# Kernel tuning notes

Hardware: AMD Instinct MI355X
Metric: run time of the kernel (lower is better)

Reference implementation:

```python
import jax, jax.numpy as jnp
import numpy as np

EPS = 1e-8

def mlp(x, w1, b1, w2, b2):
    return jnp.tanh(x @ w1 + b1) @ w2 + b2

def setup_inputs() -> dict:
    key = jax.random.key(0)
    ks = jax.random.split(key, 24)
    N_NEWS, N_USERS, N_ATR = 50000, 100000, 1000
    E_ATR, E_USR = 100000, 2000000
    D = 768
    def lin(k, fi, fo):
        return jax.random.normal(k, (fi, fo), jnp.float32) * (1.0 / np.sqrt(fi))
    inp = {
        'news_x': jax.random.normal(ks[0], (N_NEWS, D), jnp.float32),
        'users_x': jax.random.normal(ks[1], (N_USERS, 128), jnp.float32),
        'w1a': lin(ks[2], D, 256), 'b1a': jnp.zeros((256,), jnp.float32),
        'w1b': lin(ks[3], 256, 128), 'b1b': jnp.zeros((128,), jnp.float32),
        'wna': lin(ks[4], D + 128, 512), 'bna': jnp.zeros((512,), jnp.float32),
        'wnb': lin(ks[5], 512, 128), 'bnb': jnp.zeros((128,), jnp.float32),
        'wua': lin(ks[6], 256, 256), 'bua': jnp.zeros((256,), jnp.float32),
        'wub': lin(ks[7], 256, 128), 'bub': jnp.zeros((128,), jnp.float32),
        'atr_row': jax.random.randint(ks[8], (E_ATR,), 0, N_NEWS, jnp.int32),
        'atr_col': jax.random.randint(ks[9], (E_ATR,), 0, N_ATR, jnp.int32),
        'usr_row': jax.random.randint(ks[10], (E_USR,), 0, N_NEWS, jnp.int32),
        'usr_col': jax.random.randint(ks[11], (E_USR,), 0, N_USERS, jnp.int32),
        'n_news': N_NEWS, 'n_users': N_USERS, 'n_atr': N_ATR,
    }
    return inp

def reference(news_x, users_x, w1a, b1a, w1b, b1b, wna, bna, wnb, bnb,
              wua, bua, wub, bub, atr_row, atr_col, usr_row, usr_col,
              n_news, n_users, n_atr):
    dt = news_x.dtype
    ones_a = jnp.ones(atr_row.shape[0], dt)
    ones_u = jnp.ones(usr_row.shape[0], dt)
    # FirstConv: news -> attribute nodes (edge_index.t() @ news)
    deg_atr = jax.ops.segment_sum(ones_a, atr_col, num_segments=n_atr)
    agr_atr = jax.ops.segment_sum(news_x[atr_row], atr_col, num_segments=n_atr)
    agr_atr = agr_atr / (deg_atr[:, None] + EPS)
    atr_feats = mlp(agr_atr, w1a, b1a, w1b, b1b)  # [n_atr, 128]
    # NewsConv: attribute -> news (edge_index @ atr_feats), concat with news_x
    deg_news = jax.ops.segment_sum(ones_a, atr_row, num_segments=n_news)
    agr_news = jax.ops.segment_sum(atr_feats[atr_col], atr_row, num_segments=n_news)
    agr_news = agr_news / (deg_news[:, None] + EPS)
    news_out = mlp(jnp.concatenate([news_x, agr_news], axis=1), wna, bna, wnb, bnb)  # [n_news,128]
    # UserConv: news -> users (edge_index['users'].t() @ news), concat with users_x
    deg_usr = jax.ops.segment_sum(ones_u, usr_col, num_segments=n_users)
    agr_usr = jax.ops.segment_sum(news_out[usr_row], usr_col, num_segments=n_users)
    agr_usr = agr_usr / (deg_usr[:, None] + EPS)
    users_out = mlp(jnp.concatenate([users_x, agr_usr], axis=1), wua, bua, wub, bub)  # [n_users,128]
    # stack final news + user embeddings into one array
    return jnp.concatenate([news_out, users_out], axis=0)  # [n_news+n_users, 128]
```

## Files before the change

kernel.cpp:

```cpp
#include <hip/hip_runtime.h>

#define N_NEWS 50000
#define N_USERS 100000
#define N_ATR 1000
#define E_ATR 100000
#define E_USR 2000000
#define NTOT (N_ATR + N_NEWS + N_USERS)
#define EPSF 1e-8f

#define ACAP 192
#define NCAP 24
#define UCAP 64
#define FCH 8192

typedef short s16x8 __attribute__((ext_vector_type(8)));
typedef float f32x4 __attribute__((ext_vector_type(4)));

__device__ inline ushort f2bf(float f) {
    uint u = __float_as_uint(f);
    u += 0x7fffu + ((u >> 16) & 1u);
    return (ushort)(u >> 16);
}
__device__ inline float bflo(uint v) { return __uint_as_float(v << 16); }
__device__ inline float bfhi(uint v) { return __uint_as_float(v & 0xffff0000u); }
__device__ inline float fast_tanh(float x) {
    x = fminf(fmaxf(x, -15.0f), 15.0f);
    float e = __expf(2.0f * x);
    return (e - 1.0f) / (e + 1.0f);
}

struct TrJob { const float* src; ushort* dst; int R, C, blkEnd; };

struct PrepArgs {
    const int *atr_row, *atr_col, *usr_row, *usr_col;
    int *cnt_atr, *cnt_news, *cnt_usr;
    int *ids_atr, *ids_news, *ids_usr;
    const float *news_x, *users_x;
    ushort *news_bf, *users_bf;
    int fu, fa, tr, n1, n2;
    TrJob j[6];
};

__global__ void prep_k(PrepArgs A) {
    __shared__ float tile[32][33];
    int b = blockIdx.x;
    int t = threadIdx.x;
    if (b < A.fu) {
        int part = b & 7;
        int chunk = b >> 3;
        int lo = part * (N_USERS / 8), hi = lo + (N_USERS / 8);
        int base = chunk * FCH;
        int endE = base + FCH; if (endE > E_USR) endE = E_USR;
        for (int e = base + t; e < endE; e += 256) {
            int c = A.usr_col[e];
            int r = A.usr_row[e];
            if (c >= lo && c < hi) {
                int slot = atomicAdd(&A.cnt_usr[c], 1);
                if (slot < UCAP) A.ids_usr[(size_t)c * UCAP + slot] = r;
            }
        }
        return;
    }
    b -= A.fu;
    if (b < A.fa) {
        int total = 2 * E_ATR;
        int per = (total + A.fa - 1) / A.fa;
        int base = b * per;
        int endE = base + per; if (endE > total) endE = total;
        for (int e = base + t; e < endE; e += 256) {
            if (e < E_ATR) {
                int c = A.atr_col[e];
                int slot = atomicAdd(&A.cnt_atr[c], 1);
                if (slot < ACAP) A.ids_atr[(size_t)c * ACAP + slot] = A.atr_row[e];
            } else {
                int e2 = e - E_ATR;
                int r = A.atr_row[e2];
                int slot = atomicAdd(&A.cnt_news[r], 1);
                if (slot < NCAP) A.ids_news[(size_t)r * NCAP + slot] = A.atr_col[e2];
            }
        }
        return;
    }
    b -= A.fa;
    if (b < A.tr) {
        int ji = 0;
        while (b >= A.j[ji].blkEnd) ++ji;
        const TrJob& J = A.j[ji];
        int lb = b - (ji ? A.j[ji - 1].blkEnd : 0);
        int ctiles = J.C / 32;
        int bc = (lb % ctiles) * 32, br = (lb / ctiles) * 32;
        int tx = t & 31, ty = t >> 5;
        for (int i = 0; i < 4; ++i)
            tile[ty + i * 8][tx] = J.src[(size_t)(br + ty + i * 8) * J.C + bc + tx];
        __syncthreads();
        for (int i = 0; i < 4; ++i)
            J.dst[(size_t)(bc + ty + i * 8) * J.R + br + tx] = f2bf(tile[tx][ty + i * 8]);
        return;
    }
    b -= A.tr;
    int i = b * 256 + t;
    const float* src; ushort* dst;
    if (i < A.n1) { src = A.news_x; dst = A.news_bf; }
    else          { i -= A.n1; if (i >= A.n2) return; src = A.users_x; dst = A.users_bf; }
    const float4* p = (const float4*)src + (size_t)i * 2;
    float4 a = p[0], c4 = p[1];
    uint4 v;
    v.x = (uint)f2bf(a.x) | ((uint)f2bf(a.y) << 16);
    v.y = (uint)f2bf(a.z) | ((uint)f2bf(a.w) << 16);
    v.z = (uint)f2bf(c4.x) | ((uint)f2bf(c4.y) << 16);
    v.w = (uint)f2bf(c4.z) | ((uint)f2bf(c4.w) << 16);
    ((uint4*)dst)[i] = v;
}

__global__ void gather768b_k(const ushort* __restrict__ src, const int* __restrict__ ids,
                             const int* __restrict__ cnt, ushort* __restrict__ agr_b) {
    int u = blockIdx.x;
    int t = threadIdx.x;
    int dc = cnt[u];
    int d = dc < ACAP ? dc : ACAP;
    const int* bp = ids + (size_t)u * ACAP;
    float a0 = 0.f, a1 = 0.f, a2 = 0.f, a3 = 0.f;
    int i = 0;
    for (; i + 3 < d; i += 4) {
        const uint* r0 = (const uint*)(src + (size_t)bp[i] * 768);
        const uint* r1 = (const uint*)(src + (size_t)bp[i + 1] * 768);
        const uint* r2 = (const uint*)(src + (size_t)bp[i + 2] * 768);
        const uint* r3 = (const uint*)(src + (size_t)bp[i + 3] * 768);
        uint v0 = r0[t], v1 = r1[t], v2 = r2[t], v3 = r3[t];
        a0 += bflo(v0) + bflo(v1) + bflo(v2) + bflo(v3);
        a1 += bfhi(v0) + bfhi(v1) + bfhi(v2) + bfhi(v3);
        if (t < 128) {
            uint w0 = r0[t + 256], w1 = r1[t + 256], w2 = r2[t + 256], w3 = r3[t + 256];
            a2 += bflo(w0) + bflo(w1) + bflo(w2) + bflo(w3);
            a3 += bfhi(w0) + bfhi(w1) + bfhi(w2) + bfhi(w3);
        }
    }
    for (; i < d; ++i) {
        const uint* r0 = (const uint*)(src + (size_t)bp[i] * 768);
        uint v0 = r0[t];
        a0 += bflo(v0); a1 += bfhi(v0);
        if (t < 128) {
            uint v1 = r0[t + 256];
            a2 += bflo(v1); a3 += bfhi(v1);
        }
    }
    float inv = 1.0f / ((float)dc + EPSF);
    uint* dst = (uint*)(agr_b + (size_t)u * 768);
    dst[t] = (uint)f2bf(a0 * inv) | ((uint)f2bf(a1 * inv) << 16);
    if (t < 128)
        dst[256 + t] = (uint)f2bf(a2 * inv) | ((uint)f2bf(a3 * inv) << 16);
}

template<int CAP>
__global__ void gather128c_k(const ushort* __restrict__ srcp, const int* __restrict__ ids,
                             const int* __restrict__ cnt, ushort* __restrict__ agr, int n) {
    int u = blockIdx.x * 4 + (threadIdx.x >> 6);
    if (u >= n) return;
    int lane = threadIdx.x & 63;
    int dc = cnt[u];
    int d = dc < CAP ? dc : CAP;
    const int* bp = ids + (size_t)u * CAP;
    float ax = 0.f, ay = 0.f;
    int i = 0;
    for (; i + 3 < d; i += 4) {
        int s0 = bp[i], s1 = bp[i + 1], s2 = bp[i + 2], s3 = bp[i + 3];
        uint v0 = ((const uint*)srcp)[(size_t)s0 * 64 + lane];
        uint v1 = ((const uint*)srcp)[(size_t)s1 * 64 + lane];
        uint v2 = ((const uint*)srcp)[(size_t)s2 * 64 + lane];
        uint v3 = ((const uint*)srcp)[(size_t)s3 * 64 + lane];
        ax += bflo(v0) + bflo(v1) + bflo(v2) + bflo(v3);
        ay += bfhi(v0) + bfhi(v1) + bfhi(v2) + bfhi(v3);
    }
    for (; i < d; ++i) {
        uint v0 = ((const uint*)srcp)[(size_t)bp[i] * 64 + lane];
        ax += bflo(v0); ay += bfhi(v0);
    }
    float inv = 1.0f / ((float)dc + EPSF);
    uint packed = (uint)f2bf(ax * inv) | ((uint)f2bf(ay * inv) << 16);
    *(uint*)(agr + (size_t)u * 128 + lane * 2) = packed;
}

template<int NS, int NS1, bool TANH, int OMODE, int GY>
__launch_bounds__(256, 3)
__global__ void gemm5_k(const ushort* __restrict__ A1, const ushort* __restrict__ A2,
                        const ushort* __restrict__ Bt, const float* __restrict__ bias,
                        float* __restrict__ outf, ushort* __restrict__ outb,
                        int M, int N) {
    __shared__ __align__(16) char lds[32768];
    const int t = threadIdx.x;
    const int w = t >> 6, l = t & 63, lr = l & 15, lk = l >> 4;
    const int wm = w >> 1, wn = w & 1;
    int nwg = gridDim.x;
    int q = nwg >> 3, r = nwg & 7;
    int xcd = blockIdx.x & 7, idx = blockIdx.x >> 3;
    int fid = (xcd < r) ? xcd * (q + 1) + idx : r * (q + 1) + (xcd - r) * q + idx;
    constexpr int LG = (GY == 4) ? 2 : (GY == 2) ? 1 : 0;
    const int row0 = (fid >> LG) * 128;
    const int col0 = (fid & (GY - 1)) * 128;
    constexpr int A1RB = NS1 * 128;
    constexpr int A2RB = (NS - NS1) * 128;
    constexpr int BRB = NS * 128;

    auto stage = [&](int s) {
        const char* abase; int arb, soff;
        if (s < NS1) { abase = (const char*)A1; arb = A1RB; soff = s * 128; }
        else         { abase = (const char*)A2; arb = A2RB; soff = (s - NS1) * 128; }
#pragma unroll
        for (int i = 0; i < 4; ++i) {
            int chunk = i * 256 + w * 64 + l;
            int row = chunk >> 3, sub = chunk & 7;
            int rg = row0 + row; if (rg >= M) rg = M - 1;
            const char* src = abase + (size_t)rg * arb + soff + ((sub * 16) ^ ((row & 7) << 4));
            __builtin_amdgcn_global_load_lds(
                (const __attribute__((address_space(1))) unsigned int*)src,
                (__attribute__((address_space(3))) unsigned int*)(lds + i * 4096 + w * 1024),
                16, 0, 0);
        }
#pragma unroll
        for (int i = 0; i < 4; ++i) {
            int chunk = i * 256 + w * 64 + l;
            int row = chunk >> 3, sub = chunk & 7;
            const char* src = (const char*)Bt + (size_t)(col0 + row) * BRB + s * 128
                              + ((sub * 16) ^ ((row & 7) << 4));
            __builtin_amdgcn_global_load_lds(
                (const __attribute__((address_space(1))) unsigned int*)src,
                (__attribute__((address_space(3))) unsigned int*)(lds + 16384 + i * 4096 + w * 1024),
                16, 0, 0);
        }
    };

    f32x4 acc[4][4];
#pragma unroll
    for (int i = 0; i < 4; ++i)
#pragma unroll
        for (int j = 0; j < 4; ++j) acc[i][j] = (f32x4)0.f;

    stage(0);
    for (int s = 0; s < NS; ++s) {
        __syncthreads();
#pragma unroll
        for (int ks = 0; ks < 2; ++ks) {
            s16x8 af[4], bf[4];
#pragma unroll
            for (int rt = 0; rt < 4; ++rt) {
                int rr = wm * 64 + rt * 16 + lr;
                af[rt] = *(const s16x8*)(lds + rr * 128 + ((ks * 64 + lk * 16) ^ ((rr & 7) << 4)));
            }
#pragma unroll
            for (int ct = 0; ct < 4; ++ct) {
                int c = wn * 64 + ct * 16 + lr;
                bf[ct] = *(const s16x8*)(lds + 16384 + c * 128 + ((ks * 64 + lk * 16) ^ ((c & 7) << 4)));
            }
#pragma unroll
            for (int rt = 0; rt < 4; ++rt)
#pragma unroll
                for (int ct = 0; ct < 4; ++ct)
                    acc[rt][ct] = __builtin_amdgcn_mfma_f32_16x16x32_bf16(
                        af[rt], bf[ct], acc[rt][ct], 0, 0, 0);
        }
        __syncthreads();
        if (s + 1 < NS) stage(s + 1);
    }

    if (OMODE == 0) {
#pragma unroll
        for (int rt = 0; rt < 4; ++rt)
#pragma unroll
            for (int ct = 0; ct < 4; ++ct) {
                int c = wn * 64 + ct * 16 + lr;
                float bs = bias[col0 + c];
#pragma unroll
                for (int r4 = 0; r4 < 4; ++r4) {
                    int rr = wm * 64 + rt * 16 + lk * 4 + r4;
                    float v = acc[rt][ct][r4] + bs;
                    if (TANH) v = fast_tanh(v);
                    *(ushort*)(lds + rr * 256 + ((c * 2) ^ ((rr & 7) << 4))) = f2bf(v);
                }
            }
        __syncthreads();
#pragma unroll
        for (int i = 0; i < 8; ++i) {
            int chunk = i * 256 + t;
            int rr = chunk >> 4, cb = (chunk & 15) * 16;
            int rg = row0 + rr;
            if (rg < M)
                *(float4*)((char*)outb + (size_t)rg * (N * 2) + col0 * 2 + cb) =
                    *(const float4*)(lds + rr * 256 + (cb ^ ((rr & 7) << 4)));
        }
    } else {
#pragma unroll
        for (int rt = 0; rt < 4; ++rt)
#pragma unroll
            for (int ct = 0; ct < 4; ++ct) {
                int c = col0 + wn * 64 + ct * 16 + lr;
                float bs = bias[c];
#pragma unroll
                for (int r4 = 0; r4 < 4; ++r4) {
                    int rg = row0 + wm * 64 + rt * 16 + lk * 4 + r4;
                    if (rg < M) {
                        float v = acc[rt][ct][r4] + bs;
                        if (TANH) v = fast_tanh(v);
                        outf[(size_t)rg * N + c] = v;
                        if (OMODE == 2) outb[(size_t)rg * N + c] = f2bf(v);
                    }
                }
            }
    }
}

extern "C" void kernel_launch(void* const* d_in, const int* in_sizes, int n_in,
                              void* d_out, int out_size, void* d_ws, size_t ws_size,
                              hipStream_t stream) {
    const float* news_x  = (const float*)d_in[0];
    const float* users_x = (const float*)d_in[1];
    const float* w1a = (const float*)d_in[2];
    const float* b1a = (const float*)d_in[3];
    const float* w1b = (const float*)d_in[4];
    const float* b1b = (const float*)d_in[5];
    const float* wna = (const float*)d_in[6];
    const float* bna = (const float*)d_in[7];
    const float* wnb = (const float*)d_in[8];
    const float* bnb = (const float*)d_in[9];
    const float* wua = (const float*)d_in[10];
    const float* bua = (const float*)d_in[11];
    const float* wub = (const float*)d_in[12];
    const float* bub = (const float*)d_in[13];
    const int* atr_row = (const int*)d_in[14];
    const int* atr_col = (const int*)d_in[15];
    const int* usr_row = (const int*)d_in[16];
    const int* usr_col = (const int*)d_in[17];

    char* ws = (char*)d_ws;
    size_t o = 0;
    auto alloc = [&](size_t bytes) { void* p = ws + o; o += (bytes + 255) & ~(size_t)255; return p; };

    int* cnt_all = (int*)alloc((size_t)NTOT * 4);
    size_t zero_bytes = o;
    int* cnt_atr  = cnt_all;
    int* cnt_news = cnt_all + N_ATR;
    int* cnt_usr  = cnt_all + N_ATR + N_NEWS;
    int* ids_atr  = (int*)alloc((size_t)N_ATR * ACAP * 4);
    int* ids_news = (int*)alloc((size_t)N_NEWS * NCAP * 4);
    int* ids_usr  = (int*)alloc((size_t)N_USERS * UCAP * 4);
    ushort* news_bf    = (ushort*)alloc((size_t)N_NEWS * 768 * 2);
    ushort* users_bf   = (ushort*)alloc((size_t)N_USERS * 128 * 2);
    ushort* agr_atr_b  = (ushort*)alloc((size_t)N_ATR * 768 * 2);
    ushort* h_atr_b    = (ushort*)alloc((size_t)N_ATR * 256 * 2);
    ushort* atr_feats_b= (ushort*)alloc((size_t)N_ATR * 128 * 2);
    ushort* agr_news_b = (ushort*)alloc((size_t)N_NEWS * 128 * 2);
    ushort* agr_usr_b  = (ushort*)alloc((size_t)N_USERS * 128 * 2);
    ushort* out_news_b = (ushort*)alloc((size_t)N_NEWS * 128 * 2);
    ushort* h_buf      = (ushort*)alloc((size_t)N_USERS * 256 * 2);
    ushort* w1at = (ushort*)alloc((size_t)256 * 768 * 2);
    ushort* w1bt = (ushort*)alloc((size_t)128 * 256 * 2);
    ushort* wnat = (ushort*)alloc((size_t)512 * 896 * 2);
    ushort* wnbt = (ushort*)alloc((size_t)128 * 512 * 2);
    ushort* wuat = (ushort*)alloc((size_t)256 * 256 * 2);
    ushort* wubt = (ushort*)alloc((size_t)128 * 256 * 2);

    float* out = (float*)d_out;
    float* out_users = out + (size_t)N_NEWS * 128;

    hipMemsetAsync(cnt_all, 0, zero_bytes, stream);

    {
        PrepArgs A;
        A.atr_row = atr_row; A.atr_col = atr_col;
        A.usr_row = usr_row; A.usr_col = usr_col;
        A.cnt_atr = cnt_atr; A.cnt_news = cnt_news; A.cnt_usr = cnt_usr;
        A.ids_atr = ids_atr; A.ids_news = ids_news; A.ids_usr = ids_usr;
        A.news_x = news_x; A.users_x = users_x;
        A.news_bf = news_bf; A.users_bf = users_bf;
        A.fu = ((E_USR + FCH - 1) / FCH) * 8;
        A.fa = 25;
        A.n1 = N_NEWS * 768 / 8;
        A.n2 = N_USERS * 128 / 8;
        int acc2 = 0;
        auto add = [&](int i, const float* s, ushort* d, int R, int C) {
            acc2 += (C / 32) * (R / 32);
            A.j[i] = TrJob{s, d, R, C, acc2};
        };
        add(0, w1a, w1at, 768, 256);
        add(1, w1b, w1bt, 256, 128);
        add(2, wna, wnat, 896, 512);
        add(3, wnb, wnbt, 512, 128);
        add(4, wua, wuat, 256, 256);
        add(5, wub, wubt, 256, 128);
        A.tr = acc2;
        int cvt_blk = (A.n1 + A.n2 + 255) / 256;
        prep_k<<<A.fu + A.fa + A.tr + cvt_blk, 256, 0, stream>>>(A);
    }

    gather768b_k<<<N_ATR, 256, 0, stream>>>(news_bf, ids_atr, cnt_atr, agr_atr_b);
    gemm5_k<12, 12, true, 0, 2><<<16, 256, 0, stream>>>(
        agr_atr_b, nullptr, w1at, b1a, nullptr, h_atr_b, N_ATR, 256);
    gemm5_k<4, 4, false, 0, 1><<<8, 256, 0, stream>>>(
        h_atr_b, nullptr, w1bt, b1b, nullptr, atr_feats_b, N_ATR, 128);
    gather128c_k<NCAP><<<(N_NEWS + 3) / 4, 256, 0, stream>>>(
        atr_feats_b, ids_news, cnt_news, agr_news_b, N_NEWS);

    gemm5_k<14, 12, true, 0, 4><<<391 * 4, 256, 0, stream>>>(
        news_bf, agr_news_b, wnat, bna, nullptr, h_buf, N_NEWS, 512);
    gemm5_k<8, 8, false, 2, 1><<<391, 256, 0, stream>>>(
        h_buf, nullptr, wnbt, bnb, out, out_news_b, N_NEWS, 128);

    gather128c_k<UCAP><<<(N_USERS + 3) / 4, 256, 0, stream>>>(
        out_news_b, ids_usr, cnt_usr, agr_usr_b, N_USERS);
    gemm5_k<4, 2, true, 0, 2><<<782 * 2, 256, 0, stream>>>(
        users_bf, agr_usr_b, wuat, bua, nullptr, h_buf, N_USERS, 256);
    gemm5_k<4, 4, false, 1, 1><<<782, 256, 0, stream>>>(
        h_buf, nullptr, wubt, bub, out_users, nullptr, N_USERS, 128);
}
```

Before: 468.3 us.

## Replace per-user atomic bucketing with two-level partitioned CSR build for user edges

The user-edge bucketing no longer scans all 2M edges eight times with a global atomic per user. Edges are first binned into 250 partitions using block-local shared-memory counters, with one global atomic per partition per block. A new mid kernel then counting-sorts each partition into a compact CSR (start/count), and runs alongside the 768-wide attribute gather. This cuts redundant edge reads and global atomic contention, but adds a packed 64-bit arena pass and an extra kernel phase, and relies on a fixed per-partition capacity.

```diff
diff --git a/kernel.cpp b/kernel.cpp
--- a/kernel.cpp
+++ b/kernel.cpp
@@ -5,13 +5,14 @@
 #define N_ATR 1000
 #define E_ATR 100000
 #define E_USR 2000000
-#define NTOT (N_ATR + N_NEWS + N_USERS)
 #define EPSF 1e-8f
 
 #define ACAP 192
 #define NCAP 24
-#define UCAP 64
-#define FCH 8192
+#define P_USR 250
+#define UPP 400
+#define ACAPP 9216
+#define EBLK_A 8192
 
 typedef short s16x8 __attribute__((ext_vector_type(8)));
 typedef float f32x4 __attribute__((ext_vector_type(4)));
@@ -33,35 +34,46 @@
 
 struct PrepArgs {
     const int *atr_row, *atr_col, *usr_row, *usr_col;
-    int *cnt_atr, *cnt_news, *cnt_usr;
-    int *ids_atr, *ids_news, *ids_usr;
+    int *cnt_atr, *cnt_news, *arena_cnt;
+    int *ids_atr, *ids_news;
+    unsigned long long* arena;
     const float *news_x, *users_x;
     ushort *news_bf, *users_bf;
-    int fu, fa, tr, n1, n2;
+    int pa, fa, tr, n1, n2;
     TrJob j[6];
 };
 
 __global__ void prep_k(PrepArgs A) {
     __shared__ float tile[32][33];
+    __shared__ int cloc[P_USR], cbase[P_USR];
     int b = blockIdx.x;
     int t = threadIdx.x;
-    if (b < A.fu) {
-        int part = b & 7;
-        int chunk = b >> 3;
-        int lo = part * (N_USERS / 8), hi = lo + (N_USERS / 8);
-        int base = chunk * FCH;
-        int endE = base + FCH; if (endE > E_USR) endE = E_USR;
+    if (b < A.pa) {
+        if (t < P_USR) cloc[t] = 0;
+        __syncthreads();
+        int base = b * EBLK_A;
+        int endE = base + EBLK_A; if (endE > E_USR) endE = E_USR;
+        for (int e = base + t; e < endE; e += 256)
+            atomicAdd(&cloc[A.usr_col[e] / UPP], 1);
+        __syncthreads();
+        if (t < P_USR) {
+            cbase[t] = atomicAdd(&A.arena_cnt[t], cloc[t]);
+            cloc[t] = 0;
+        }
+        __syncthreads();
         for (int e = base + t; e < endE; e += 256) {
             int c = A.usr_col[e];
             int r = A.usr_row[e];
-            if (c >= lo && c < hi) {
-                int slot = atomicAdd(&A.cnt_usr[c], 1);
-                if (slot < UCAP) A.ids_usr[(size_t)c * UCAP + slot] = r;
-            }
+            int p = c / UPP;
+            int off = atomicAdd(&cloc[p], 1);
+            int slot = cbase[p] + off;
+            if (slot < ACAPP)
+                A.arena[(size_t)p * ACAPP + slot] =
+                    ((unsigned long long)(uint)c << 32) | (uint)r;
         }
         return;
     }
-    b -= A.fu;
+    b -= A.pa;
     if (b < A.fa) {
         int total = 2 * E_ATR;
         int per = (total + A.fa - 1) / A.fa;
@@ -112,13 +124,61 @@
     ((uint4*)dst)[i] = v;
 }
 
-__global__ void gather768b_k(const ushort* __restrict__ src, const int* __restrict__ ids,
-                             const int* __restrict__ cnt, ushort* __restrict__ agr_b) {
-    int u = blockIdx.x;
+struct MidArgs {
+    const unsigned long long* arena;
+    const int* arena_cnt;
+    int *cnt_usr, *start_usr, *ids_usr;
+    const ushort* news_bf;
+    const int* ids_atr;
+    const int* cnt_atr;
+    ushort* agr_atr_b;
+};
+
+__global__ void mid_k(MidArgs M) {
+    __shared__ int cnt[512];
+    __shared__ int scn[512];
+    int b = blockIdx.x;
     int t = threadIdx.x;
-    int dc = cnt[u];
+    if (b < P_USR) {
+        int p = b;
+        int nA = M.arena_cnt[p]; if (nA > ACAPP) nA = ACAPP;
+        const unsigned long long* ar = M.arena + (size_t)p * ACAPP;
+        cnt[t] = 0; cnt[t + 256] = 0;
+        __syncthreads();
+        for (int i = t; i < nA; i += 256)
+            atomicAdd(&cnt[(int)(ar[i] >> 32) - p * UPP], 1);
+        __syncthreads();
+        scn[t] = cnt[t]; scn[t + 256] = cnt[t + 256];
+        __syncthreads();
+        for (int off = 1; off < 512; off <<= 1) {
+            int v0 = (t >= off) ? scn[t - off] : 0;
+            int v1 = ((t + 256) >= off) ? scn[t + 256 - off] : 0;
+            __syncthreads();
+            scn[t] += v0; scn[t + 256] += v1;
+            __syncthreads();
+        }
+        for (int i = t; i < UPP; i += 256) {
+            int u = p * UPP + i;
+            M.cnt_usr[u] = cnt[i];
+            M.start_usr[u] = p * ACAPP + (scn[i] - cnt[i]);
+        }
+        __syncthreads();
+        for (int i = t; i < UPP; i += 256) cnt[i] = scn[i] - cnt[i];
+        __syncthreads();
+        for (int i = t; i < nA; i += 256) {
+            unsigned long long v = ar[i];
+            int c = (int)(v >> 32);
+            int off = atomicAdd(&cnt[c - p * UPP], 1);
+            M.ids_usr[(size_t)p * ACAPP + off] = (int)(v & 0xffffffffu);
+        }
+        return;
+    }
+    b -= P_USR;
+    int u = b;
+    int dc = M.cnt_atr[u];
     int d = dc < ACAP ? dc : ACAP;
-    const int* bp = ids + (size_t)u * ACAP;
+    const int* bp = M.ids_atr + (size_t)u * ACAP;
+    const ushort* src = M.news_bf;
     float a0 = 0.f, a1 = 0.f, a2 = 0.f, a3 = 0.f;
     int i = 0;
     for (; i + 3 < d; i += 4) {
@@ -145,7 +205,7 @@
         }
     }
     float inv = 1.0f / ((float)dc + EPSF);
-    uint* dst = (uint*)(agr_b + (size_t)u * 768);
+    uint* dst = (uint*)(M.agr_atr_b + (size_t)u * 768);
     dst[t] = (uint)f2bf(a0 * inv) | ((uint)f2bf(a1 * inv) << 16);
     if (t < 128)
         dst[256 + t] = (uint)f2bf(a2 * inv) | ((uint)f2bf(a3 * inv) << 16);
@@ -176,6 +236,34 @@
         ax += bflo(v0); ay += bfhi(v0);
     }
     float inv = 1.0f / ((float)dc + EPSF);
+    uint packed = (uint)f2bf(ax * inv) | ((uint)f2bf(ay * inv) << 16);
+    *(uint*)(agr + (size_t)u * 128 + lane * 2) = packed;
+}
+
+__global__ void gather128s_k(const ushort* __restrict__ srcp, const int* __restrict__ ids,
+                             const int* __restrict__ start, const int* __restrict__ cnt,
+                             ushort* __restrict__ agr, int n) {
+    int u = blockIdx.x * 4 + (threadIdx.x >> 6);
+    if (u >= n) return;
+    int lane = threadIdx.x & 63;
+    int d = cnt[u];
+    const int* bp = ids + start[u];
+    float ax = 0.f, ay = 0.f;
+    int i = 0;
+    for (; i + 3 < d; i += 4) {
+        int s0 = bp[i], s1 = bp[i + 1], s2 = bp[i + 2], s3 = bp[i + 3];
+        uint v0 = ((const uint*)srcp)[(size_t)s0 * 64 + lane];
+        uint v1 = ((const uint*)srcp)[(size_t)s1 * 64 + lane];
+        uint v2 = ((const uint*)srcp)[(size_t)s2 * 64 + lane];
+        uint v3 = ((const uint*)srcp)[(size_t)s3 * 64 + lane];
+        ax += bflo(v0) + bflo(v1) + bflo(v2) + bflo(v3);
+        ay += bfhi(v0) + bfhi(v1) + bfhi(v2) + bfhi(v3);
+    }
+    for (; i < d; ++i) {
+        uint v0 = ((const uint*)srcp)[(size_t)bp[i] * 64 + lane];
+        ax += bflo(v0); ay += bfhi(v0);
+    }
+    float inv = 1.0f / ((float)d + EPSF);
     uint packed = (uint)f2bf(ax * inv) | ((uint)f2bf(ay * inv) << 16);
     *(uint*)(agr + (size_t)u * 128 + lane * 2) = packed;
 }
@@ -334,14 +422,16 @@
     size_t o = 0;
     auto alloc = [&](size_t bytes) { void* p = ws + o; o += (bytes + 255) & ~(size_t)255; return p; };
 
-    int* cnt_all = (int*)alloc((size_t)NTOT * 4);
+    int* cnt_atr   = (int*)alloc(N_ATR * 4);
+    int* cnt_news  = (int*)alloc(N_NEWS * 4);
+    int* arena_cnt = (int*)alloc(P_USR * 4);
     size_t zero_bytes = o;
-    int* cnt_atr  = cnt_all;
-    int* cnt_news = cnt_all + N_ATR;
-    int* cnt_usr  = cnt_all + N_ATR + N_NEWS;
+    int* cnt_usr   = (int*)alloc((size_t)N_USERS * 4);
+    int* start_usr = (int*)alloc((size_t)N_USERS * 4);
     int* ids_atr  = (int*)alloc((size_t)N_ATR * ACAP * 4);
     int* ids_news = (int*)alloc((size_t)N_NEWS * NCAP * 4);
-    int* ids_usr  = (int*)alloc((size_t)N_USERS * UCAP * 4);
+    int* ids_usr  = (int*)alloc((size_t)P_USR * ACAPP * 4);
+    unsigned long long* arena = (unsigned long long*)alloc((size_t)P_USR * ACAPP * 8);
     ushort* news_bf    = (ushort*)alloc((size_t)N_NEWS * 768 * 2);
     ushort* users_bf   = (ushort*)alloc((size_t)N_USERS * 128 * 2);
     ushort* agr_atr_b  = (ushort*)alloc((size_t)N_ATR * 768 * 2);
@@ -361,17 +451,18 @@
     float* out = (float*)d_out;
     float* out_users = out + (size_t)N_NEWS * 128;
 
-    hipMemsetAsync(cnt_all, 0, zero_bytes, stream);
+    hipMemsetAsync(cnt_atr, 0, zero_bytes, stream);
 
     {
         PrepArgs A;
         A.atr_row = atr_row; A.atr_col = atr_col;
         A.usr_row = usr_row; A.usr_col = usr_col;
-        A.cnt_atr = cnt_atr; A.cnt_news = cnt_news; A.cnt_usr = cnt_usr;
-        A.ids_atr = ids_atr; A.ids_news = ids_news; A.ids_usr = ids_usr;
+        A.cnt_atr = cnt_atr; A.cnt_news = cnt_news; A.arena_cnt = arena_cnt;
+        A.ids_atr = ids_atr; A.ids_news = ids_news;
+        A.arena = arena;
         A.news_x = news_x; A.users_x = users_x;
         A.news_bf = news_bf; A.users_bf = users_bf;
-        A.fu = ((E_USR + FCH - 1) / FCH) * 8;
+        A.pa = (E_USR + EBLK_A - 1) / EBLK_A;
         A.fa = 25;
         A.n1 = N_NEWS * 768 / 8;
         A.n2 = N_USERS * 128 / 8;
@@ -388,10 +479,18 @@
         add(5, wub, wubt, 256, 128);
         A.tr = acc2;
         int cvt_blk = (A.n1 + A.n2 + 255) / 256;
-        prep_k<<<A.fu + A.fa + A.tr + cvt_blk, 256, 0, stream>>>(A);
-    }
-
-    gather768b_k<<<N_ATR, 256, 0, stream>>>(news_bf, ids_atr, cnt_atr, agr_atr_b);
+        prep_k<<<A.pa + A.fa + A.tr + cvt_blk, 256, 0, stream>>>(A);
+    }
+
+    {
+        MidArgs M;
+        M.arena = arena; M.arena_cnt = arena_cnt;
+        M.cnt_usr = cnt_usr; M.start_usr = start_usr; M.ids_usr = ids_usr;
+        M.news_bf = news_bf; M.ids_atr = ids_atr; M.cnt_atr = cnt_atr;
+        M.agr_atr_b = agr_atr_b;
+        mid_k<<<P_USR + N_ATR, 256, 0, stream>>>(M);
+    }
+
     gemm5_k<12, 12, true, 0, 2><<<16, 256, 0, stream>>>(
         agr_atr_b, nullptr, w1at, b1a, nullptr, h_atr_b, N_ATR, 256);
     gemm5_k<4, 4, false, 0, 1><<<8, 256, 0, stream>>>(
@@ -404,8 +503,8 @@
     gemm5_k<8, 8, false, 2, 1><<<391, 256, 0, stream>>>(
         h_buf, nullptr, wnbt, bnb, out, out_news_b, N_NEWS, 128);
 
-    gather128c_k<UCAP><<<(N_USERS + 3) / 4, 256, 0, stream>>>(
-        out_news_b, ids_usr, cnt_usr, agr_usr_b, N_USERS);
+    gather128s_k<<<(N_USERS + 3) / 4, 256, 0, stream>>>(
+        out_news_b, ids_usr, start_usr, cnt_usr, agr_usr_b, N_USERS);
     gemm5_k<4, 2, true, 0, 2><<<782 * 2, 256, 0, stream>>>(
         users_bf, agr_usr_b, wuat, bua, nullptr, h_buf, N_USERS, 256);
     gemm5_k<4, 4, false, 1, 1><<<782, 256, 0, stream>>>(
```

Measured after the change: 422.4 us. 1.11x faster.
